# Optimization experiments

Hardware: AMD Instinct MI355X
Metric: run time of the kernel (lower is better)

## Reference

```python
import jax, jax.numpy as jnp
import numpy as np

NL, D, DI, N, R, K = 32, 256, 512, 16, 16, 4   # layers, d_model, d_inner, d_state, dt_rank, d_conv
V, FF, BATCH, L = 4096, 1024, 32, 256


def _mamba_layer(x, p):
    # x: (B, L, D). One pre-norm Mamba block with residual: x + mamba(LN(x)).
    ln_w, ln_b, in_w, cw, cb, xp_w, dtw, dtb, A_log, Dskip, out_w = p
    mu = x.mean(-1, keepdims=True)
    var = ((x - mu) ** 2).mean(-1, keepdims=True)
    h = (x - mu) / jnp.sqrt(var + 1e-5) * ln_w + ln_b
    xz = jnp.einsum('bld,ed->ble', h, in_w)            # (B, L, 2*DI)
    xm, z = jnp.split(xz, 2, axis=-1)
    seq = xm.shape[1]
    # causal depthwise conv1d, kernel K, then SiLU
    xpad = jnp.pad(xm, ((0, 0), (K - 1, 0), (0, 0)))
    xc = sum(xpad[:, k:k + seq] * cw[:, k] for k in range(K)) + cb
    xc = jax.nn.silu(xc)
    dbc = jnp.einsum('ble,fe->blf', xc, xp_w)          # (B, L, R+2N)
    dt, Bm, Cm = jnp.split(dbc, [R, R + N], axis=-1)
    dt = jax.nn.softplus(jnp.einsum('blr,er->ble', dt, dtw) + dtb)  # (B, L, DI)
    A = -jnp.exp(A_log)                                # (DI, N)

    def step(hs, inp):
        dt_t, B_t, C_t, x_t = inp                      # (B,DI),(B,N),(B,N),(B,DI)
        dA = jnp.exp(dt_t[..., None] * A)              # (B, DI, N)
        hs = hs * dA + (dt_t * x_t)[..., None] * B_t[:, None, :]
        return hs, jnp.einsum('ben,bn->be', hs, C_t)

    h0 = jnp.zeros((xc.shape[0], DI, N), xc.dtype)
    _, ys = jax.lax.scan(step, h0, (dt.swapaxes(0, 1), Bm.swapaxes(0, 1), Cm.swapaxes(0, 1), xc.swapaxes(0, 1)))
    y = ys.swapaxes(0, 1) + xc * Dskip
    y = y * jax.nn.silu(z)
    return x + jnp.einsum('ble,de->bld', y, out_w)


def _stack_forward(x, params):
    return jax.lax.scan(lambda c, p: (jax.checkpoint(_mamba_layer)(c, p), None), x, params)[0]


def setup_inputs() -> dict:
    key = jax.random.key(0)
    ks = jax.random.split(key, 12)
    rn = lambda k, shape, s=0.02: jax.random.normal(k, shape, jnp.float32) * s
    return {
        'token_ids': jax.random.randint(ks[0], (BATCH, L), 0, V),
        'emb': rn(ks[1], (V, D)),
        'ln_w': jnp.ones((NL, D)), 'ln_b': jnp.zeros((NL, D)),
        'in_proj_w': rn(ks[2], (NL, 2 * DI, D)),
        'conv_w': rn(ks[3], (NL, DI, K), 0.1), 'conv_b': jnp.zeros((NL, DI)),
        'x_proj_w': rn(ks[4], (NL, R + 2 * N, DI)),
        'dt_w': rn(ks[5], (NL, DI, R), 0.1),
        'dt_b': jnp.full((NL, DI), float(np.log(np.expm1(0.01))), jnp.float32),
        'A_log': jnp.broadcast_to(jnp.log(jnp.arange(1, N + 1, dtype=jnp.float32)), (NL, DI, N)) + 0.0,
        'Dskip': jnp.ones((NL, DI)),
        'out_proj_w': rn(ks[6], (NL, D, DI)),
        'W1': rn(ks[7], (FF, D)), 'b1': jnp.zeros((FF,)),
        'W2': rn(ks[8], (V, FF)), 'b2': jnp.zeros((V,)),
    }


def reference(token_ids, emb, ln_w, ln_b, in_proj_w, conv_w, conv_b, x_proj_w, dt_w, dt_b, A_log, Dskip, out_proj_w, W1, b1, W2, b2):
    x = emb[token_ids]                                  # (B, L, D)
    params = (ln_w, ln_b, in_proj_w, conv_w, conv_b, x_proj_w, dt_w, dt_b, A_log, Dskip, out_proj_w)
    x = _stack_forward(x, params)                       # 32 stacked Mamba blocks
    h = jax.nn.relu(x @ W1.T + b1)
    return h @ W2.T + b2                                # (B, L, V) logits
```

## Files before the change

### kernel.cpp

```cpp
#include <hip/hip_runtime.h>
#include <hip/hip_bf16.h>
#include <cstdint>
#include <cstddef>


typedef __bf16 v8bf __attribute__((ext_vector_type(8)));
typedef float  v4f  __attribute__((ext_vector_type(4)));

__device__ __forceinline__ void async_copy16(const void* g, void* l) {
  __builtin_amdgcn_global_load_lds((const __attribute__((address_space(1))) void*)g,
                                   (__attribute__((address_space(3))) void*)l, 16, 0, 0);
}

__device__ __forceinline__ float bf(__bf16 v) { return (float)v; }

constexpr size_t OFF_WIN  = 0;
constexpr size_t OFF_WXP  = 16777216;
constexpr size_t OFF_WOUT = 18350080;
constexpr size_t OFF_WW1  = 26738688;
constexpr size_t OFF_WW2  = 27262976;
constexpr size_t OFF_X    = 35651584;
constexpr size_t OFF_H    = 44040192;
constexpr size_t OFF_XC   = 48234496;
constexpr size_t OFF_DBC  = 65011712;
constexpr size_t OFF_PART = 66584576;
constexpr size_t OFF_SS   = 82313216;
constexpr size_t OFF_A2   = 83296256;

__global__ __launch_bounds__(256)
void f2b_multi(const float* __restrict__ s0, const float* __restrict__ s1,
               const float* __restrict__ s2, const float* __restrict__ s3,
               const float* __restrict__ s4, const float* __restrict__ s5,
               char* __restrict__ ws) {
  size_t i = (size_t)blockIdx.x * 256 + threadIdx.x;
  if (i < 8388608) { ((__bf16*)(ws + OFF_WIN))[i] = (__bf16)s0[i]; return; }
  i -= 8388608;
  if (i < 786432)  { ((__bf16*)(ws + OFF_WXP))[i] = (__bf16)s1[i]; return; }
  i -= 786432;
  if (i < 4194304) { ((__bf16*)(ws + OFF_WOUT))[i] = (__bf16)s2[i]; return; }
  i -= 4194304;
  if (i < 262144)  { ((__bf16*)(ws + OFF_WW1))[i] = (__bf16)s3[i]; return; }
  i -= 262144;
  if (i < 4194304) { ((__bf16*)(ws + OFF_WW2))[i] = (__bf16)s4[i]; return; }
  i -= 4194304;
  ((float*)(ws + OFF_A2))[i] = -1.4426950408889634f * __expf(s5[i]);
}

__global__ __launch_bounds__(256) void f2b_k(const float* __restrict__ X,
                                             __bf16* __restrict__ O) {
  size_t i = (size_t)blockIdx.x * 256 + threadIdx.x;
  O[i] = (__bf16)X[i];
}

__global__ __launch_bounds__(256)
void embed_ln_k(const int* __restrict__ tok, const float* __restrict__ emb,
                const float* __restrict__ w, const float* __restrict__ b,
                float* __restrict__ X, __bf16* __restrict__ H) {
  int row = blockIdx.x;
  int t   = threadIdx.x;
  float v = emb[(size_t)tok[row] * 256 + t];
  X[(size_t)row * 256 + t] = v;
  float s = v, q = v * v;
  #pragma unroll
  for (int o = 32; o > 0; o >>= 1) { s += __shfl_xor(s, o); q += __shfl_xor(q, o); }
  __shared__ float ss[4], qq[4];
  int wv = t >> 6;
  if ((t & 63) == 0) { ss[wv] = s; qq[wv] = q; }
  __syncthreads();
  s = ss[0] + ss[1] + ss[2] + ss[3];
  q = qq[0] + qq[1] + qq[2] + qq[3];
  float mu  = s * (1.f / 256.f);
  float var = q * (1.f / 256.f) - mu * mu;
  float r   = rsqrtf(var + 1e-5f);
  H[(size_t)row * 256 + t] = (__bf16)((v - mu) * r * w[t] + b[t]);
}

template <int EPI>
__global__ __launch_bounds__(256, 2)
void gemm_bt(const __bf16* __restrict__ A, const __bf16* __restrict__ W,
             void* outp, const float* __restrict__ bias, int M, int N, int K) {
  __shared__ __align__(16) __bf16 sA[128 * 32];
  __shared__ __align__(16) __bf16 sB[128 * 32];
  const int tid  = threadIdx.x;
  const int bm0  = blockIdx.y << 7;
  const int bn0  = blockIdx.x << 7;
  const int lane = tid & 63;
  const int wv   = tid >> 6;
  const int wm   = (wv >> 1) << 6;
  const int wn   = (wv & 1) << 6;
  const int lr   = lane & 15;
  const int lk   = lane >> 4;

  v4f acc[4][4] = {};

  const int r0 = tid >> 2;
  const int c0 = (tid & 3) << 3;
  const int wbase = (tid & ~63) << 3;

  const __bf16* gA0 = A + (size_t)(bm0 + r0) * K + c0;
  const __bf16* gA1 = A + (size_t)(bm0 + 64 + r0) * K + c0;
  const __bf16* gB0 = W + (size_t)(bn0 + r0) * K + c0;
  const __bf16* gB1 = W + (size_t)(bn0 + 64 + r0) * K + c0;

  for (int kk = 0; kk < K; kk += 32) {
    async_copy16(gA0 + kk, sA + wbase);
    async_copy16(gA1 + kk, sA + 2048 + wbase);
    async_copy16(gB0 + kk, sB + wbase);
    async_copy16(gB1 + kk, sB + 2048 + wbase);
    __syncthreads();
    v8bf af[4], bfr[4];
    #pragma unroll
    for (int i = 0; i < 4; ++i)
      af[i] = *(const v8bf*)(sA + ((wm + i * 16 + lr) << 5) + (lk << 3));
    #pragma unroll
    for (int j = 0; j < 4; ++j)
      bfr[j] = *(const v8bf*)(sB + ((wn + j * 16 + lr) << 5) + (lk << 3));
    #pragma unroll
    for (int i = 0; i < 4; ++i)
      #pragma unroll
      for (int j = 0; j < 4; ++j)
        acc[i][j] = __builtin_amdgcn_mfma_f32_16x16x32_bf16(af[i], bfr[j], acc[i][j], 0, 0, 0);
    __syncthreads();
  }

  #pragma unroll
  for (int i = 0; i < 4; ++i) {
    #pragma unroll
    for (int j = 0; j < 4; ++j) {
      int gc = bn0 + wn + j * 16 + lr;
      #pragma unroll
      for (int v = 0; v < 4; ++v) {
        int gr = bm0 + wm + i * 16 + (lk << 2) + v;
        float val = acc[i][j][v];
        size_t idx = (size_t)gr * N + gc;
        if (EPI == 0) {
          ((__bf16*)outp)[idx] = (__bf16)val;
        } else if (EPI == 1) {
          val += bias[gc]; val = fmaxf(val, 0.f);
          ((__bf16*)outp)[idx] = (__bf16)val;
        } else {
          ((float*)outp)[idx] = val + bias[gc];
        }
      }
    }
  }
}

__global__ __launch_bounds__(512, 2)
void k2_inconv_k(const __bf16* __restrict__ H, const __bf16* __restrict__ Wi,
                 const float* __restrict__ cw, const float* __restrict__ cb,
                 const __bf16* __restrict__ Wxp,
                 const float* __restrict__ dtw, const float* __restrict__ dtb,
                 const float* __restrict__ A2,
                 __bf16* __restrict__ XC, float* __restrict__ DBC,
                 float* __restrict__ PART, float* __restrict__ SS) {
  __shared__ __align__(16) char sm[93184];
  __bf16* const sH   = (__bf16*)sm;
  __bf16* const sB   = (__bf16*)(sm + 24576);
  __bf16* const sXM  = (__bf16*)(sm + 57344);
  __bf16* const sXC  = (__bf16*)(sm + 24576);
  float*  const sDBC = (float*)sm;

  const int tid = threadIdx.x;
  const int c   = blockIdx.x >> 5;
  const int b   = blockIdx.x & 31;
  const int bl0 = b * 256 + c * 32;
  const int lane = tid & 63, wv = tid >> 6;
  const int lr = lane & 15, lk = lane >> 4;

  #pragma unroll
  for (int rnd = 0; rnd < 3; ++rnd) {
    const int q = rnd * 512 + tid;
    if (q < 1120) {
      const int row = q >> 5, cc = q & 31;
      int hr = bl0 - 3 + row; if (hr < 0) hr = 0;
      const v8bf hv = *(const v8bf*)(H + (size_t)hr * 256 + (cc << 3));
      *(v8bf*)(sH + row * 256 + ((cc ^ (row & 7)) << 3)) = hv;
    }
  }
  __syncthreads();

  const int wn = wv << 6;
  {
    v4f acc[3][4] = {};
    for (int kk = 0; kk < 256; kk += 32) {
      #pragma unroll
      for (int rnd = 0; rnd < 4; ++rnd) {
        const int q = rnd * 512 + tid;
        const int n = q >> 2, cbs = (q & 3) ^ (n & 3);
        async_copy16(Wi + (size_t)n * 256 + kk + (cbs << 3), sB + ((q & ~63) << 3));
      }
      __syncthreads();
      v8bf af[3], bfr[4];
      #pragma unroll
      for (int i = 0; i < 3; ++i) {
        const int row = i * 16 + lr;
        af[i] = *(const v8bf*)(sH + row * 256 + ((((kk >> 3) + lk) ^ (row & 7)) << 3));
      }
      #pragma unroll
      for (int j = 0; j < 4; ++j) {
        const int n = wn + j * 16 + lr;
        bfr[j] = *(const v8bf*)(sB + n * 32 + ((lk ^ (n & 3)) << 3));
      }
      #pragma unroll
      for (int i = 0; i < 3; ++i)
        #pragma unroll
        for (int j = 0; j < 4; ++j)
          acc[i][j] = __builtin_amdgcn_mfma_f32_16x16x32_bf16(af[i], bfr[j], acc[i][j], 0, 0, 0);
      __syncthreads();
    }
    #pragma unroll
    for (int i = 0; i < 3; ++i)
      #pragma unroll
      for (int v = 0; v < 4; ++v) {
        const int row = i * 16 + (lk << 2) + v;
        if (row < 35) {
          #pragma unroll
          for (int j = 0; j < 4; ++j) {
            float val = acc[i][j][v];
            if (c == 0 && row < 3) val = 0.f;
            sXM[row * 512 + wn + j * 16 + lr] = (__bf16)val;
          }
        }
      }
  }
  __syncthreads();

  {
    const int r = tid >> 4, ec = tid & 15;
    #pragma unroll
    for (int j = 0; j < 4; ++j) {
      const int e = (ec << 3) + (j << 7);
      v4f cw4[8];
      #pragma unroll
      for (int jj = 0; jj < 8; ++jj) cw4[jj] = *(const v4f*)(cw + (size_t)(e + jj) * 4);
      float a[8];
      #pragma unroll
      for (int jj = 0; jj < 8; ++jj) a[jj] = cb[e + jj];
      #pragma unroll
      for (int k = 0; k < 4; ++k) {
        const v8bf xv = *(const v8bf*)(sXM + (r + k) * 512 + e);
        #pragma unroll
        for (int jj = 0; jj < 8; ++jj) a[jj] += bf(xv[jj]) * cw4[jj][k];
      }
      v8bf outv;
      #pragma unroll
      for (int jj = 0; jj < 8; ++jj) {
        const float s = a[jj] / (1.f + __expf(-a[jj]));
        outv[jj] = (__bf16)s;
      }
      const int cbk = (e >> 3) ^ (r & 7);
      *(v8bf*)(sXC + r * 512 + (cbk << 3)) = outv;
      *(v8bf*)(XC + (size_t)(bl0 + r) * 512 + e) = outv;
    }
  }
  __syncthreads();

  if (tid < 192) {
    const int w = tid >> 6;
    v4f accp[2] = {};
    for (int kk = 0; kk < 512; kk += 32) {
      const v8bf bfr = *(const v8bf*)(Wxp + (size_t)(w * 16 + lr) * 512 + kk + (lk << 3));
      #pragma unroll
      for (int i = 0; i < 2; ++i) {
        const int row = i * 16 + lr;
        const int cbk = (((kk >> 3) + lk) ^ (row & 7));
        const v8bf af = *(const v8bf*)(sXC + row * 512 + (cbk << 3));
        accp[i] = __builtin_amdgcn_mfma_f32_16x16x32_bf16(af, bfr, accp[i], 0, 0, 0);
      }
    }
    const int gc = w * 16 + lr;
    #pragma unroll
    for (int i = 0; i < 2; ++i)
      #pragma unroll
      for (int v = 0; v < 4; ++v)
        sDBC[(i * 16 + (lk << 2) + v) * 48 + gc] = accp[i][v];
  }
  __syncthreads();

  if (tid < 384)
    *(v4f*)(DBC + (size_t)bl0 * 48 + tid * 4) = *(const v4f*)(sDBC + tid * 4);

  if (c < 7) {
    const int e = tid;
    v4f a2v[4], wd[4];
    #pragma unroll
    for (int q = 0; q < 4; ++q) {
      a2v[q] = *(const v4f*)(A2  + (size_t)e * 16 + q * 4);
      wd[q]  = *(const v4f*)(dtw + (size_t)e * 16 + q * 4);
    }
    const float bias = dtb[e];
    float part[16];
    #pragma unroll
    for (int n = 0; n < 16; ++n) part[n] = 0.f;
    float S = 0.f;
    for (int tt = 0; tt < 32; ++tt) {
      const v4f* dp = (const v4f*)(sDBC + tt * 48);
      float dtv = bias;
      {
        const v4f d0 = dp[0], d1 = dp[1], d2 = dp[2], d3 = dp[3];
        #pragma unroll
        for (int r2 = 0; r2 < 4; ++r2)
          dtv += d0[r2] * wd[0][r2] + d1[r2] * wd[1][r2] + d2[r2] * wd[2][r2] + d3[r2] * wd[3][r2];
      }
      dtv = (dtv > 20.f) ? dtv : log1pf(__expf(dtv));
      const float x = bf(sXC[tt * 512 + (((e >> 3) ^ (tt & 7)) << 3) + (e & 7)]);
      const float dtx = dtv * x;
      S += dtv;
      {
        const v4f bv0 = dp[4], bv1 = dp[5], bv2 = dp[6], bv3 = dp[7];
        #pragma unroll
        for (int v = 0; v < 4; ++v) {
          part[v]      = part[v]      * exp2f(dtv * a2v[0][v]) + dtx * bv0[v];
          part[4 + v]  = part[4 + v]  * exp2f(dtv * a2v[1][v]) + dtx * bv1[v];
          part[8 + v]  = part[8 + v]  * exp2f(dtv * a2v[2][v]) + dtx * bv2[v];
          part[12 + v] = part[12 + v] * exp2f(dtv * a2v[3][v]) + dtx * bv3[v];
        }
      }
    }
    const size_t o = (((size_t)c * 32 + b) * 512 + e) * 16;
    #pragma unroll
    for (int rq = 0; rq < 4; ++rq) {
      v4f p;
      #pragma unroll
      for (int v = 0; v < 4; ++v) p[v] = part[rq * 4 + v];
      *(v4f*)(PART + o + rq * 4) = p;
    }
    SS[((size_t)c * 32 + b) * 512 + e] = S;
  }
}

__global__ __launch_bounds__(512, 2)
void k3_zscan_k(const __bf16* H, const __bf16* __restrict__ Wz,
                const __bf16* __restrict__ XC, const float* __restrict__ DBC,
                const float* __restrict__ dtw, const float* __restrict__ dtb,
                const float* __restrict__ A2, const float* __restrict__ Dskip,
                const float* __restrict__ PART, const float* __restrict__ SS,
                const __bf16* __restrict__ Wout,
                const float* __restrict__ lnw, const float* __restrict__ lnb,
                float* __restrict__ X, __bf16* Hout) {
  __shared__ __align__(16) char sm[83968];
  __bf16* const sH   = (__bf16*)sm;
  __bf16* const sBz  = (__bf16*)(sm + 16384);
  __bf16* const sY   = (__bf16*)sm;
  __bf16* const sB3  = (__bf16*)(sm + 33280);
  float*  const sSum = (float*)(sm + 49664);
  float*  const sSq  = (float*)(sm + 50176);
  __bf16* const sZ   = (__bf16*)(sm + 50688);

  const int tid = threadIdx.x;
  const int c   = blockIdx.x >> 5;
  const int b   = blockIdx.x & 31;
  const int bl0 = b * 256 + c * 32;
  const int lane = tid & 63, wv = tid >> 6;
  const int lr = lane & 15, lk = lane >> 4;

  #pragma unroll
  for (int rnd = 0; rnd < 2; ++rnd) {
    const int q = rnd * 512 + tid;
    const int row = q >> 5, cc = q & 31;
    const v8bf hv = *(const v8bf*)(H + (size_t)(bl0 + row) * 256 + (cc << 3));
    *(v8bf*)(sH + row * 256 + ((cc ^ (row & 7)) << 3)) = hv;
  }
  __syncthreads();

  const int wn = wv << 6;
  {
    v4f acc[2][4] = {};
    for (int kk = 0; kk < 256; kk += 32) {
      #pragma unroll
      for (int rnd = 0; rnd < 4; ++rnd) {
        const int q = rnd * 512 + tid;
        const int n = q >> 2, cbs = (q & 3) ^ (n & 3);
        async_copy16(Wz + (size_t)n * 256 + kk + (cbs << 3), sBz + ((q & ~63) << 3));
      }
      __syncthreads();
      v8bf af[2], bfr[4];
      #pragma unroll
      for (int i = 0; i < 2; ++i) {
        const int row = i * 16 + lr;
        af[i] = *(const v8bf*)(sH + row * 256 + ((((kk >> 3) + lk) ^ (row & 7)) << 3));
      }
      #pragma unroll
      for (int j = 0; j < 4; ++j) {
        const int n = wn + j * 16 + lr;
        bfr[j] = *(const v8bf*)(sBz + n * 32 + ((lk ^ (n & 3)) << 3));
      }
      #pragma unroll
      for (int i = 0; i < 2; ++i)
        #pragma unroll
        for (int j = 0; j < 4; ++j)
          acc[i][j] = __builtin_amdgcn_mfma_f32_16x16x32_bf16(af[i], bfr[j], acc[i][j], 0, 0, 0);
      __syncthreads();
    }
    #pragma unroll
    for (int i = 0; i < 2; ++i)
      #pragma unroll
      for (int v = 0; v < 4; ++v) {
        const int row = i * 16 + (lk << 2) + v;
        #pragma unroll
        for (int j = 0; j < 4; ++j)
          sZ[row * 520 + wn + j * 16 + lr] = (__bf16)acc[i][j][v];
      }
  }
  __syncthreads();

  const int e = tid;
  v4f a2v[4], wd[4];
  #pragma unroll
  for (int q = 0; q < 4; ++q) {
    a2v[q] = *(const v4f*)(A2  + (size_t)e * 16 + q * 4);
    wd[q]  = *(const v4f*)(dtw + (size_t)e * 16 + q * 4);
  }
  const float bias = dtb[e];
  const float Dsk  = Dskip[e];
  float h[16];
  #pragma unroll
  for (int n = 0; n < 16; ++n) h[n] = 0.f;
  for (int cc = 0; cc < c; ++cc) {
    const float S  = SS[((size_t)cc * 32 + b) * 512 + e];
    const size_t o = (((size_t)cc * 32 + b) * 512 + e) * 16;
    #pragma unroll
    for (int rq = 0; rq < 4; ++rq) {
      const v4f p = *(const v4f*)(PART + o + rq * 4);
      #pragma unroll
      for (int v = 0; v < 4; ++v)
        h[rq * 4 + v] = h[rq * 4 + v] * exp2f(a2v[rq][v] * S) + p[v];
    }
  }

  for (int tt = 0; tt < 32; ++tt) {
    const float x = bf(XC[(size_t)(bl0 + tt) * 512 + e]);
    const v4f* dp = (const v4f*)(DBC + (size_t)(bl0 + tt) * 48);
    float dtv = bias;
    {
      const v4f d0 = dp[0], d1 = dp[1], d2 = dp[2], d3 = dp[3];
      #pragma unroll
      for (int r2 = 0; r2 < 4; ++r2)
        dtv += d0[r2] * wd[0][r2] + d1[r2] * wd[1][r2] + d2[r2] * wd[2][r2] + d3[r2] * wd[3][r2];
    }
    dtv = (dtv > 20.f) ? dtv : log1pf(__expf(dtv));
    const float dtx = dtv * x;
    float y = 0.f;
    {
      const v4f bv0 = dp[4], bv1 = dp[5], bv2 = dp[6], bv3 = dp[7];
      const v4f cv0 = dp[8], cv1 = dp[9], cv2 = dp[10], cv3 = dp[11];
      #pragma unroll
      for (int v = 0; v < 4; ++v) {
        h[v]      = h[v]      * exp2f(dtv * a2v[0][v]) + dtx * bv0[v];  y += h[v]      * cv0[v];
        h[4 + v]  = h[4 + v]  * exp2f(dtv * a2v[1][v]) + dtx * bv1[v];  y += h[4 + v]  * cv1[v];
        h[8 + v]  = h[8 + v]  * exp2f(dtv * a2v[2][v]) + dtx * bv2[v];  y += h[8 + v]  * cv2[v];
        h[12 + v] = h[12 + v] * exp2f(dtv * a2v[3][v]) + dtx * bv3[v];  y += h[12 + v] * cv3[v];
      }
    }
    const float z  = bf(sZ[tt * 520 + e]);
    const float sg = z / (1.f + __expf(-z));
    sY[tt * 520 + e] = (__bf16)((y + x * Dsk) * sg);
  }
  __syncthreads();

  const int wm = (wv & 1) << 4;
  const int wn3 = (wv >> 1) << 6;
  v4f acc3[4] = {};
  for (int kk = 0; kk < 512; kk += 32) {
    async_copy16(Wout + (size_t)(tid >> 2) * 512 + ((tid & 3) << 3) + kk,
                 sB3 + ((tid & ~63) << 3));
    async_copy16(Wout + (size_t)(128 + (tid >> 2)) * 512 + ((tid & 3) << 3) + kk,
                 sB3 + 4096 + ((tid & ~63) << 3));
    __syncthreads();
    const v8bf af = *(const v8bf*)(sY + (wm + lr) * 520 + kk + (lk << 3));
    #pragma unroll
    for (int j = 0; j < 4; ++j) {
      const v8bf bfr = *(const v8bf*)(sB3 + ((wn3 + j * 16 + lr) << 5) + (lk << 3));
      acc3[j] = __builtin_amdgcn_mfma_f32_16x16x32_bf16(af, bfr, acc3[j], 0, 0, 0);
    }
    __syncthreads();
  }

  float s2[4], q2[4];
  #pragma unroll
  for (int v = 0; v < 4; ++v) {
    const int gr = bl0 + wm + (lk << 2) + v;
    float s = 0.f, q = 0.f;
    #pragma unroll
    for (int j = 0; j < 4; ++j) {
      const int gc = wn3 + j * 16 + lr;
      float val = X[(size_t)gr * 256 + gc] + acc3[j][v];
      acc3[j][v] = val;
      s += val; q += val * val;
    }
    #pragma unroll
    for (int o = 8; o > 0; o >>= 1) { s += __shfl_xor(s, o); q += __shfl_xor(q, o); }
    s2[v] = s; q2[v] = q;
  }
  if (lr == 0) {
    #pragma unroll
    for (int v = 0; v < 4; ++v) {
      const int row = wm + (lk << 2) + v;
      sSum[(wv >> 1) * 32 + row] = s2[v];
      sSq[(wv >> 1) * 32 + row]  = q2[v];
    }
  }
  __syncthreads();
  #pragma unroll
  for (int v = 0; v < 4; ++v) {
    const int row = wm + (lk << 2) + v;
    const float S = sSum[row] + sSum[32 + row] + sSum[64 + row] + sSum[96 + row];
    const float Q = sSq[row]  + sSq[32 + row]  + sSq[64 + row]  + sSq[96 + row];
    const float mu   = S * (1.f / 256.f);
    const float var  = Q * (1.f / 256.f) - mu * mu;
    const float rinv = rsqrtf(var + 1e-5f);
    const int gr = bl0 + row;
    #pragma unroll
    for (int j = 0; j < 4; ++j) {
      const int gc = wn3 + j * 16 + lr;
      const float val = acc3[j][v];
      X[(size_t)gr * 256 + gc] = val;
      Hout[(size_t)gr * 256 + gc] = (__bf16)((val - mu) * rinv * lnw[gc] + lnb[gc]);
    }
  }
}

extern "C" void kernel_launch(void* const* d_in, const int* in_sizes, int n_in,
                              void* d_out, int out_size, void* d_ws, size_t ws_size,
                              hipStream_t stream) {
  const int*   tok  = (const int*)d_in[0];
  const float* emb  = (const float*)d_in[1];
  const float* lnw  = (const float*)d_in[2];
  const float* lnb  = (const float*)d_in[3];
  const float* inw  = (const float*)d_in[4];
  const float* cw   = (const float*)d_in[5];
  const float* cb   = (const float*)d_in[6];
  const float* xpw  = (const float*)d_in[7];
  const float* dtw  = (const float*)d_in[8];
  const float* dtb  = (const float*)d_in[9];
  const float* alog = (const float*)d_in[10];
  const float* dsk  = (const float*)d_in[11];
  const float* outw = (const float*)d_in[12];
  const float* W1   = (const float*)d_in[13];
  const float* b1   = (const float*)d_in[14];
  const float* W2   = (const float*)d_in[15];
  const float* b2   = (const float*)d_in[16];

  char* ws = (char*)d_ws;
  __bf16* WIN   = (__bf16*)(ws + OFF_WIN);
  __bf16* WXP   = (__bf16*)(ws + OFF_WXP);
  __bf16* WOUT  = (__bf16*)(ws + OFF_WOUT);
  __bf16* WW1   = (__bf16*)(ws + OFF_WW1);
  __bf16* WW2   = (__bf16*)(ws + OFF_WW2);
  float*  X     = (float*)(ws + OFF_X);
  __bf16* H     = (__bf16*)(ws + OFF_H);
  __bf16* XC    = (__bf16*)(ws + OFF_XC);
  float*  DBC   = (float*)(ws + OFF_DBC);
  float*  PART  = (float*)(ws + OFF_PART);
  float*  SS    = (float*)(ws + OFF_SS);
  float*  A2    = (float*)(ws + OFF_A2);
  __bf16* XB    = (__bf16*)(ws + OFF_PART);
  __bf16* HH    = (__bf16*)(ws + OFF_PART + 8388608);

  f2b_multi<<<70656, 256, 0, stream>>>(inw, xpw, outw, W1, W2, alog, ws);
  embed_ln_k<<<8192, 256, 0, stream>>>(tok, emb, lnw, lnb, X, H);

  for (int l = 0; l < 32; ++l) {
    const __bf16* Wi_l   = WIN  + (size_t)l * 262144;
    const __bf16* Wz_l   = WIN  + (size_t)l * 262144 + 131072;
    const float*  cw_l   = cw   + (size_t)l * 2048;
    const float*  cb_l   = cb   + (size_t)l * 512;
    const __bf16* xpw_l  = WXP  + (size_t)l * 24576;
    const float*  dtw_l  = dtw  + (size_t)l * 8192;
    const float*  dtb_l  = dtb  + (size_t)l * 512;
    const float*  A2_l   = A2   + (size_t)l * 8192;
    const float*  dsk_l  = dsk  + (size_t)l * 512;
    const __bf16* outw_l = WOUT + (size_t)l * 131072;
    const int lnx = (l + 1 < 32) ? l + 1 : 31;

    k2_inconv_k<<<256, 512, 0, stream>>>(H, Wi_l, cw_l, cb_l, xpw_l, dtw_l, dtb_l,
                                         A2_l, XC, DBC, PART, SS);
    k3_zscan_k<<<256, 512, 0, stream>>>(H, Wz_l, XC, DBC, dtw_l, dtb_l, A2_l,
                                        dsk_l, PART, SS, outw_l,
                                        lnw + (size_t)lnx * 256,
                                        lnb + (size_t)lnx * 256, X, H);
  }

  f2b_k<<<8192, 256, 0, stream>>>(X, XB);
  gemm_bt<1><<<dim3(8, 64), 256, 0, stream>>>(XB, WW1, HH, b1, 8192, 1024, 256);
  gemm_bt<2><<<dim3(32, 64), 256, 0, stream>>>(HH, WW2, (float*)d_out, b2, 8192, 4096, 1024);
}
```

Baseline: 4.126 ms.

## Swizzle LDS tiles by row pairs and stage scan inputs in LDS

Changes the XOR swizzle on the 32-wide bf16 LDS tiles in gemm_bt, the in-proj kernel and both GEMMs of k3_zscan_k from (row&3) to ((row>>1)&3), with matching global source addresses, to cut LDS bank conflicts on the 16-byte MFMA operand reads. It also prefetches the block's XC and DBC slices into LDS with async copies at kernel start, so the sequential scan loop reads shared memory instead of issuing global loads every step. LDS use in k3 rises to about 120 KB, which may limit how many blocks fit per CU despite launch_bounds(512,2).

```diff
diff --git a/kernel.cpp b/kernel.cpp
--- a/kernel.cpp
+++ b/kernel.cpp
@@ -94,7 +94,7 @@
   v4f acc[4][4] = {};
 
   const int r0 = tid >> 2;
-  const int c0 = (tid & 3) << 3;
+  const int c0 = (((tid & 3) ^ ((r0 >> 1) & 3)) << 3);
   const int wbase = (tid & ~63) << 3;
 
   const __bf16* gA0 = A + (size_t)(bm0 + r0) * K + c0;
@@ -110,11 +110,15 @@
     __syncthreads();
     v8bf af[4], bfr[4];
     #pragma unroll
-    for (int i = 0; i < 4; ++i)
-      af[i] = *(const v8bf*)(sA + ((wm + i * 16 + lr) << 5) + (lk << 3));
-    #pragma unroll
-    for (int j = 0; j < 4; ++j)
-      bfr[j] = *(const v8bf*)(sB + ((wn + j * 16 + lr) << 5) + (lk << 3));
+    for (int i = 0; i < 4; ++i) {
+      const int row = wm + i * 16 + lr;
+      af[i] = *(const v8bf*)(sA + (row << 5) + ((lk ^ ((row >> 1) & 3)) << 3));
+    }
+    #pragma unroll
+    for (int j = 0; j < 4; ++j) {
+      const int row = wn + j * 16 + lr;
+      bfr[j] = *(const v8bf*)(sB + (row << 5) + ((lk ^ ((row >> 1) & 3)) << 3));
+    }
     #pragma unroll
     for (int i = 0; i < 4; ++i)
       #pragma unroll
@@ -187,7 +191,7 @@
       #pragma unroll
       for (int rnd = 0; rnd < 4; ++rnd) {
         const int q = rnd * 512 + tid;
-        const int n = q >> 2, cbs = (q & 3) ^ (n & 3);
+        const int n = q >> 2, cbs = (q & 3) ^ ((n >> 1) & 3);
         async_copy16(Wi + (size_t)n * 256 + kk + (cbs << 3), sB + ((q & ~63) << 3));
       }
       __syncthreads();
@@ -200,7 +204,7 @@
       #pragma unroll
       for (int j = 0; j < 4; ++j) {
         const int n = wn + j * 16 + lr;
-        bfr[j] = *(const v8bf*)(sB + n * 32 + ((lk ^ (n & 3)) << 3));
+        bfr[j] = *(const v8bf*)(sB + n * 32 + ((lk ^ ((n >> 1) & 3)) << 3));
       }
       #pragma unroll
       for (int i = 0; i < 3; ++i)
@@ -339,14 +343,16 @@
                 const __bf16* __restrict__ Wout,
                 const float* __restrict__ lnw, const float* __restrict__ lnb,
                 float* __restrict__ X, __bf16* Hout) {
-  __shared__ __align__(16) char sm[83968];
-  __bf16* const sH   = (__bf16*)sm;
-  __bf16* const sBz  = (__bf16*)(sm + 16384);
-  __bf16* const sY   = (__bf16*)sm;
-  __bf16* const sB3  = (__bf16*)(sm + 33280);
-  float*  const sSum = (float*)(sm + 49664);
-  float*  const sSq  = (float*)(sm + 50176);
-  __bf16* const sZ   = (__bf16*)(sm + 50688);
+  __shared__ __align__(16) char sm[122880];
+  __bf16* const sH    = (__bf16*)sm;
+  __bf16* const sBz   = (__bf16*)(sm + 16384);
+  __bf16* const sY    = (__bf16*)sm;
+  __bf16* const sB3   = (__bf16*)(sm + 33280);
+  float*  const sSum  = (float*)(sm + 49664);
+  float*  const sSq   = (float*)(sm + 50176);
+  __bf16* const sZ    = (__bf16*)(sm + 50688);
+  __bf16* const sXCs  = (__bf16*)(sm + 83968);
+  float*  const sDBCs = (float*)(sm + 116736);
 
   const int tid = threadIdx.x;
   const int c   = blockIdx.x >> 5;
@@ -356,6 +362,14 @@
   const int lr = lane & 15, lk = lane >> 4;
 
   #pragma unroll
+  for (int rnd = 0; rnd < 4; ++rnd) {
+    const int m = rnd * 512 + tid;
+    async_copy16(XC + (size_t)bl0 * 512 + m * 8, sXCs + ((m & ~63) << 3));
+  }
+  if (tid < 384)
+    async_copy16(DBC + (size_t)bl0 * 48 + tid * 4, sDBCs + ((tid & ~63) << 2));
+
+  #pragma unroll
   for (int rnd = 0; rnd < 2; ++rnd) {
     const int q = rnd * 512 + tid;
     const int row = q >> 5, cc = q & 31;
@@ -371,7 +385,7 @@
       #pragma unroll
       for (int rnd = 0; rnd < 4; ++rnd) {
         const int q = rnd * 512 + tid;
-        const int n = q >> 2, cbs = (q & 3) ^ (n & 3);
+        const int n = q >> 2, cbs = (q & 3) ^ ((n >> 1) & 3);
         async_copy16(Wz + (size_t)n * 256 + kk + (cbs << 3), sBz + ((q & ~63) << 3));
       }
       __syncthreads();
@@ -384,7 +398,7 @@
       #pragma unroll
       for (int j = 0; j < 4; ++j) {
         const int n = wn + j * 16 + lr;
-        bfr[j] = *(const v8bf*)(sBz + n * 32 + ((lk ^ (n & 3)) << 3));
+        bfr[j] = *(const v8bf*)(sBz + n * 32 + ((lk ^ ((n >> 1) & 3)) << 3));
       }
       #pragma unroll
       for (int i = 0; i < 2; ++i)
@@ -430,8 +444,8 @@
   }
 
   for (int tt = 0; tt < 32; ++tt) {
-    const float x = bf(XC[(size_t)(bl0 + tt) * 512 + e]);
-    const v4f* dp = (const v4f*)(DBC + (size_t)(bl0 + tt) * 48);
+    const float x = bf(sXCs[tt * 512 + e]);
+    const v4f* dp = (const v4f*)(sDBCs + tt * 48);
     float dtv = bias;
     {
       const v4f d0 = dp[0], d1 = dp[1], d2 = dp[2], d3 = dp[3];
@@ -461,17 +475,20 @@
 
   const int wm = (wv & 1) << 4;
   const int wn3 = (wv >> 1) << 6;
+  const int nb = tid >> 2;
+  const int sw = (nb >> 1) & 3;
   v4f acc3[4] = {};
   for (int kk = 0; kk < 512; kk += 32) {
-    async_copy16(Wout + (size_t)(tid >> 2) * 512 + ((tid & 3) << 3) + kk,
+    async_copy16(Wout + (size_t)nb * 512 + (((tid & 3) ^ sw) << 3) + kk,
                  sB3 + ((tid & ~63) << 3));
-    async_copy16(Wout + (size_t)(128 + (tid >> 2)) * 512 + ((tid & 3) << 3) + kk,
+    async_copy16(Wout + (size_t)(128 + nb) * 512 + (((tid & 3) ^ sw) << 3) + kk,
                  sB3 + 4096 + ((tid & ~63) << 3));
     __syncthreads();
     const v8bf af = *(const v8bf*)(sY + (wm + lr) * 520 + kk + (lk << 3));
     #pragma unroll
     for (int j = 0; j < 4; ++j) {
-      const v8bf bfr = *(const v8bf*)(sB3 + ((wn3 + j * 16 + lr) << 5) + (lk << 3));
+      const int row = wn3 + j * 16 + lr;
+      const v8bf bfr = *(const v8bf*)(sB3 + (row << 5) + ((lk ^ ((row >> 1) & 3)) << 3));
       acc3[j] = __builtin_amdgcn_mfma_f32_16x16x32_bf16(af, bfr, acc3[j], 0, 0, 0);
     }
     __syncthreads();
```

After: 4.160 ms. No clear change (+0.8%).
